# Kernel tuning notes

Measured on AMD Instinct MI355X. Metric: run time of the kernel, lower is better.

The kernel has to match this reference:

```python
import jax, jax.numpy as jnp
import numpy as np

B, S, D, H = 4, 2048, 768, 12
DH = D // H          # 64 head dim
DF = 4 * D           # 3072 FFN hidden
EPS = 1e-5


def setup_inputs() -> dict:
    key = jax.random.key(0)
    ks = jax.random.split(key, 16)
    s = 0.02
    inp = {
        "Q": jax.random.normal(ks[0], (B, S, D), jnp.float32),
        "K": jax.random.normal(ks[1], (B, S, D), jnp.float32),
        "V": jax.random.normal(ks[2], (B, S, D), jnp.float32),
        "Wq": s * jax.random.normal(ks[3], (D, D), jnp.float32),
        "bq": jnp.zeros((D,), jnp.float32),
        "Wk": s * jax.random.normal(ks[4], (D, D), jnp.float32),
        "bk": jnp.zeros((D,), jnp.float32),
        "Wv": s * jax.random.normal(ks[5], (D, D), jnp.float32),
        "bv": jnp.zeros((D,), jnp.float32),
        "Wo": s * jax.random.normal(ks[6], (D, D), jnp.float32),
        "bo": jnp.zeros((D,), jnp.float32),
        "ln_g": jnp.ones((D,), jnp.float32),
        "ln_b": jnp.zeros((D,), jnp.float32),
        "W1": s * jax.random.normal(ks[7], (D, DF), jnp.float32),
        "b1": jnp.zeros((DF,), jnp.float32),
        "W2": s * jax.random.normal(ks[8], (DF, D), jnp.float32),
        "b2": jnp.zeros((D,), jnp.float32),
    }
    return inp


def _split_heads(x):  # [B,S,D] -> [B,H,S,DH]
    return x.reshape(B, S, H, DH).transpose(0, 2, 1, 3)


def _layernorm(x, g, b):
    mu = jnp.mean(x, axis=-1, keepdims=True)
    var = jnp.mean(jnp.square(x - mu), axis=-1, keepdims=True)
    return (x - mu) * jax.lax.rsqrt(var + EPS) * g + b


def reference(Q, K, V, Wq, bq, Wk, bk, Wv, bv, Wo, bo, ln_g, ln_b, W1, b1, W2, b2):
    q = _split_heads(Q @ Wq + bq)            # [B,H,S,DH]
    k = _split_heads(K @ Wk + bk)
    v = _split_heads(V @ Wv + bv)
    scale = 1.0 / jnp.sqrt(jnp.asarray(DH, q.dtype))
    scores = jnp.einsum("bhqd,bhkd->bhqk", q, k) * scale   # [B,H,S,S]
    attn = jax.nn.softmax(scores, axis=-1)
    ctx = jnp.einsum("bhqk,bhkd->bhqd", attn, v)            # [B,H,S,DH]
    ctx = ctx.transpose(0, 2, 1, 3).reshape(B, S, D)
    attn_out = ctx @ Wo + bo
    h = _layernorm(Q + attn_out, ln_g, ln_b)                # residual + LN
    ff = jax.nn.gelu(h @ W1 + b1, approximate=False) @ W2 + b2
    return ff
```

## Files before the change

### kernel.cpp

```cpp
#include <hip/hip_runtime.h>
#include <hip/hip_bf16.h>
#include <math.h>

#define Bsz 4
#define Ssz 2048
#define Dsz 768
#define Hn  12
#define DHn 64
#define DFn 3072
#define NTOK (Bsz*Ssz)
#define EPSL 1e-5f

typedef __attribute__((ext_vector_type(8))) short bf16x8;
typedef __attribute__((ext_vector_type(4))) float f32x4;

__device__ __forceinline__ unsigned short f2bf(float f) {
    unsigned int u = __float_as_uint(f);
    u += 0x7fffu + ((u >> 16) & 1u);
    return (unsigned short)(u >> 16);
}
__device__ __forceinline__ float bf2f(unsigned short h) {
    return __uint_as_float(((unsigned int)h) << 16);
}

__device__ __forceinline__ void swizzle_mn(int bid, int mtot, int nb, int& m, int& n)
{
    const int xcd = bid & 7;
    const int idx = bid >> 3;
    m = xcd * (mtot >> 3) + idx / nb;
    n = idx % nb;
}

__global__ __launch_bounds__(256)
void wsplit_k(const float* __restrict__ W, unsigned short* __restrict__ Wh,
              unsigned short* __restrict__ Wl, int K, int N)
{
    __shared__ float tile[32][33];
    const int n0 = blockIdx.x * 32, k0 = blockIdx.y * 32;
    const int x = threadIdx.x, y = threadIdx.y;
    #pragma unroll
    for (int i = 0; i < 4; i++)
        tile[y + 8 * i][x] = W[(size_t)(k0 + y + 8 * i) * N + n0 + x];
    __syncthreads();
    #pragma unroll
    for (int i = 0; i < 4; i++) {
        float v = tile[x][y + 8 * i];
        unsigned short hb = f2bf(v);
        size_t o = (size_t)(n0 + y + 8 * i) * K + k0 + x;
        Wh[o] = hb;
        Wl[o] = f2bf(v - bf2f(hb));
    }
}

__global__ __launch_bounds__(256)
void presplit_k(const float* __restrict__ Qf, const float* __restrict__ Kf,
                const float* __restrict__ Vf,
                unsigned short* __restrict__ Qh, unsigned short* __restrict__ Ql,
                unsigned short* __restrict__ Kh, unsigned short* __restrict__ Kl,
                unsigned short* __restrict__ Vh)
{
    const int blocksPerSeg = (NTOK * Dsz) / 2048;
    const int seg = blockIdx.x / blocksPerSeg;
    const int idx = ((blockIdx.x % blocksPerSeg) * 256 + threadIdx.x) * 8;
    const float* src = (seg == 0) ? Qf : (seg == 1) ? Kf : Vf;

    float4 a = *(const float4*)(src + idx);
    float4 b = *(const float4*)(src + idx + 4);
    float fv[8] = {a.x, a.y, a.z, a.w, b.x, b.y, b.z, b.w};

    bf16x8 h8, l8;
    #pragma unroll
    for (int e = 0; e < 8; e++) {
        unsigned short hb = f2bf(fv[e]);
        h8[e] = (short)hb;
        l8[e] = (short)f2bf(fv[e] - bf2f(hb));
    }
    unsigned short* Hp = (seg == 0) ? Qh : (seg == 1) ? Kh : Vh;
    *(bf16x8*)(Hp + idx) = h8;
    if (seg < 2) {
        unsigned short* Lp = (seg == 0) ? Ql : Kl;
        *(bf16x8*)(Lp + idx) = l8;
    }
}

__global__ __launch_bounds__(256)
void qkv_mfma(const unsigned short* __restrict__ Qsh, const unsigned short* __restrict__ Qsl,
              const unsigned short* __restrict__ Ksh, const unsigned short* __restrict__ Ksl,
              const unsigned short* __restrict__ Vsh,
              const unsigned short* __restrict__ Wqh, const unsigned short* __restrict__ Wql,
              const unsigned short* __restrict__ Wkh, const unsigned short* __restrict__ Wkl,
              const unsigned short* __restrict__ Wvh, const unsigned short* __restrict__ Wvl,
              const float* __restrict__ bq, const float* __restrict__ bk,
              const float* __restrict__ bv,
              unsigned short* __restrict__ qh, unsigned short* __restrict__ ql,
              unsigned short* __restrict__ kh, unsigned short* __restrict__ kl,
              unsigned short* __restrict__ vout)
{
    __shared__ short smem[16384];
    short* As_h = smem;
    short* As_l = smem + 4096;
    short* Bs_h = smem + 8192;
    short* Bs_l = smem + 12288;

    const int t    = threadIdx.x;
    const int lane = t & 63;
    const int w    = t >> 6;
    const int wm   = w >> 1;
    const int wn   = w & 1;

    int m_tile, nblk;
    swizzle_mn(blockIdx.x, 192, 6, m_tile, nblk);
    const int which = m_tile / 64;
    const int m0    = (m_tile % 64) * 128;
    const int n0    = nblk * 128;

    const unsigned short* Ah = (which == 0) ? Qsh : (which == 1) ? Ksh : Vsh;
    const unsigned short* Al = (which == 0) ? Qsl : Ksl;
    const unsigned short* Bh = (which == 0) ? Wqh : (which == 1) ? Wkh : Wvh;
    const unsigned short* Bl = (which == 0) ? Wql : (which == 1) ? Wkl : Wvl;
    const float* bias = (which == 0) ? bq : (which == 1) ? bk : bv;

    f32x4 acc[4][4];
    #pragma unroll
    for (int i = 0; i < 4; i++)
        #pragma unroll
        for (int j = 0; j < 4; j++)
            acc[i][j] = (f32x4){0.f, 0.f, 0.f, 0.f};

    const int fr = lane & 15;
    const int q8 = (lane >> 4) * 8;

    for (int k0 = 0; k0 < Dsz; k0 += 32) {
        __syncthreads();
        #pragma unroll
        for (int it = 0; it < 2; it++) {
            const int p   = t + 256 * it;
            const int row = p >> 2;
            const int c8  = (p & 3) * 8;
            const unsigned short* ga_h = Ah + (size_t)(m0 + row) * Dsz + k0 + c8;
            const unsigned short* gb_h = Bh + (size_t)(n0 + row) * Dsz + k0 + c8;
            __builtin_amdgcn_global_load_lds((const __attribute__((address_space(1))) void*)ga_h,
                (__attribute__((address_space(3))) void*)(As_h + p * 8), 16, 0, 0);
            __builtin_amdgcn_global_load_lds((const __attribute__((address_space(1))) void*)gb_h,
                (__attribute__((address_space(3))) void*)(Bs_h + p * 8), 16, 0, 0);
            if (which < 2) {
                const unsigned short* ga_l = Al + (size_t)(m0 + row) * Dsz + k0 + c8;
                const unsigned short* gb_l = Bl + (size_t)(n0 + row) * Dsz + k0 + c8;
                __builtin_amdgcn_global_load_lds((const __attribute__((address_space(1))) void*)ga_l,
                    (__attribute__((address_space(3))) void*)(As_l + p * 8), 16, 0, 0);
                __builtin_amdgcn_global_load_lds((const __attribute__((address_space(1))) void*)gb_l,
                    (__attribute__((address_space(3))) void*)(Bs_l + p * 8), 16, 0, 0);
            }
        }
        __syncthreads();

        bf16x8 a_h[4], a_l[4], b_h[4], b_l[4];
        #pragma unroll
        for (int i = 0; i < 4; i++) {
            const int ra = (wm * 64 + i * 16 + fr) * 32 + q8;
            const int rb = (wn * 64 + i * 16 + fr) * 32 + q8;
            a_h[i] = *(const bf16x8*)&As_h[ra];
            b_h[i] = *(const bf16x8*)&Bs_h[rb];
            if (which < 2) {
                a_l[i] = *(const bf16x8*)&As_l[ra];
                b_l[i] = *(const bf16x8*)&Bs_l[rb];
            }
        }
        if (which < 2) {
            #pragma unroll
            for (int i = 0; i < 4; i++)
                #pragma unroll
                for (int j = 0; j < 4; j++) {
                    acc[i][j] = __builtin_amdgcn_mfma_f32_16x16x32_bf16(a_l[i], b_h[j], acc[i][j], 0, 0, 0);
                    acc[i][j] = __builtin_amdgcn_mfma_f32_16x16x32_bf16(a_h[i], b_l[j], acc[i][j], 0, 0, 0);
                    acc[i][j] = __builtin_amdgcn_mfma_f32_16x16x32_bf16(a_h[i], b_h[j], acc[i][j], 0, 0, 0);
                }
        } else {
            #pragma unroll
            for (int i = 0; i < 4; i++)
                #pragma unroll
                for (int j = 0; j < 4; j++)
                    acc[i][j] = __builtin_amdgcn_mfma_f32_16x16x32_bf16(a_h[i], b_h[j], acc[i][j], 0, 0, 0);
        }
    }

    const int quad = lane >> 4;
    #pragma unroll
    for (int i = 0; i < 4; i++)
        #pragma unroll
        for (int j = 0; j < 4; j++) {
            const int n  = n0 + wn * 64 + j * 16 + fr;
            const float bn = bias[n];
            const int hh = n >> 6, dh = n & 63;
            #pragma unroll
            for (int r = 0; r < 4; r++) {
                const int m = m0 + wm * 64 + i * 16 + quad * 4 + r;
                const int bb = m >> 11, s = m & 2047;
                const size_t o = (((size_t)bb * Hn + hh) * Ssz + s) * DHn + dh;
                float v = acc[i][j][r] + bn;
                unsigned short hb = f2bf(v);
                if (which == 0) { qh[o] = hb; ql[o] = f2bf(v - bf2f(hb)); }
                else if (which == 1) { kh[o] = hb; kl[o] = f2bf(v - bf2f(hb)); }
                else vout[o] = hb;
            }
        }
}

__global__ __launch_bounds__(256)
void vtrans_k(const unsigned short* __restrict__ src, unsigned short* __restrict__ dst)
{
    __shared__ unsigned short tl[32][33];
    const int s0 = blockIdx.x * 32;
    const int d0 = blockIdx.y * 32;
    const int hd = blockIdx.z;
    const int x = threadIdx.x, y = threadIdx.y;
    const size_t base = (size_t)hd * Ssz * DHn;
    #pragma unroll
    for (int i = 0; i < 4; i++)
        tl[y + 8 * i][x] = src[base + (size_t)(s0 + y + 8 * i) * DHn + d0 + x];
    __syncthreads();
    #pragma unroll
    for (int i = 0; i < 4; i++)
        dst[base + (size_t)(d0 + y + 8 * i) * Ssz + s0 + x] = tl[x][y + 8 * i];
}

template<int MODE, bool ASPLIT, bool BSPLIT>
__global__ __launch_bounds__(256)
void gemm_mfma(const unsigned short* __restrict__ Ah, const unsigned short* __restrict__ Al,
               const unsigned short* __restrict__ Bh, const unsigned short* __restrict__ Bl,
               const float* __restrict__ bias, const float* __restrict__ res,
               float* __restrict__ Cf, unsigned short* __restrict__ Cb,
               int M, int N, int K)
{
    __shared__ short smem[16384];
    short* As_h = smem;
    short* As_l = smem + 4096;
    short* Bs_h = smem + 8192;
    short* Bs_l = smem + 12288;

    const int t    = threadIdx.x;
    const int lane = t & 63;
    const int w    = t >> 6;
    const int wm   = w >> 1;
    const int wn   = w & 1;

    int mt, nt_;
    swizzle_mn(blockIdx.x, M >> 7, N >> 7, mt, nt_);
    const int m0 = mt * 128;
    const int n0 = nt_ * 128;

    f32x4 acc[4][4];
    #pragma unroll
    for (int i = 0; i < 4; i++)
        #pragma unroll
        for (int j = 0; j < 4; j++)
            acc[i][j] = (f32x4){0.f, 0.f, 0.f, 0.f};

    const int fr = lane & 15;
    const int q8 = (lane >> 4) * 8;

    for (int k0 = 0; k0 < K; k0 += 32) {
        __syncthreads();
        #pragma unroll
        for (int it = 0; it < 2; it++) {
            const int p   = t + 256 * it;
            const int row = p >> 2;
            const int c8  = (p & 3) * 8;
            const unsigned short* ga_h = Ah + (size_t)(m0 + row) * K + k0 + c8;
            const unsigned short* gb_h = Bh + (size_t)(n0 + row) * K + k0 + c8;
            __builtin_amdgcn_global_load_lds((const __attribute__((address_space(1))) void*)ga_h,
                (__attribute__((address_space(3))) void*)(As_h + p * 8), 16, 0, 0);
            if (ASPLIT) {
                const unsigned short* ga_l = Al + (size_t)(m0 + row) * K + k0 + c8;
                __builtin_amdgcn_global_load_lds((const __attribute__((address_space(1))) void*)ga_l,
                    (__attribute__((address_space(3))) void*)(As_l + p * 8), 16, 0, 0);
            }
            __builtin_amdgcn_global_load_lds((const __attribute__((address_space(1))) void*)gb_h,
                (__attribute__((address_space(3))) void*)(Bs_h + p * 8), 16, 0, 0);
            if (BSPLIT) {
                const unsigned short* gb_l = Bl + (size_t)(n0 + row) * K + k0 + c8;
                __builtin_amdgcn_global_load_lds((const __attribute__((address_space(1))) void*)gb_l,
                    (__attribute__((address_space(3))) void*)(Bs_l + p * 8), 16, 0, 0);
            }
        }
        __syncthreads();

        bf16x8 a_h[4], a_l[4], b_h[4], b_l[4];
        #pragma unroll
        for (int i = 0; i < 4; i++) {
            const int ra = (wm * 64 + i * 16 + fr) * 32 + q8;
            const int rb = (wn * 64 + i * 16 + fr) * 32 + q8;
            a_h[i] = *(const bf16x8*)&As_h[ra];
            if (ASPLIT) a_l[i] = *(const bf16x8*)&As_l[ra];
            b_h[i] = *(const bf16x8*)&Bs_h[rb];
            if (BSPLIT) b_l[i] = *(const bf16x8*)&Bs_l[rb];
        }
        #pragma unroll
        for (int i = 0; i < 4; i++)
            #pragma unroll
            for (int j = 0; j < 4; j++) {
                if (ASPLIT)
                    acc[i][j] = __builtin_amdgcn_mfma_f32_16x16x32_bf16(a_l[i], b_h[j], acc[i][j], 0, 0, 0);
                if (BSPLIT)
                    acc[i][j] = __builtin_amdgcn_mfma_f32_16x16x32_bf16(a_h[i], b_l[j], acc[i][j], 0, 0, 0);
                acc[i][j] = __builtin_amdgcn_mfma_f32_16x16x32_bf16(a_h[i], b_h[j], acc[i][j], 0, 0, 0);
            }
    }

    const int quad = lane >> 4;
    #pragma unroll
    for (int i = 0; i < 4; i++)
        #pragma unroll
        for (int j = 0; j < 4; j++) {
            const int n  = n0 + wn * 64 + j * 16 + fr;
            const float bn = bias[n];
            #pragma unroll
            for (int r = 0; r < 4; r++) {
                const int m = m0 + wm * 64 + i * 16 + quad * 4 + r;
                float v = acc[i][j][r] + bn;
                if (MODE == 1) {
                    v += res[(size_t)m * N + n];
                    Cf[(size_t)m * N + n] = v;
                } else if (MODE == 2) {
                    v = 0.5f * v * (1.0f + erff(v * 0.70710678118654752f));
                    Cb[(size_t)m * N + n] = f2bf(v);
                } else {
                    Cf[(size_t)m * N + n] = v;
                }
            }
        }
}

__device__ __forceinline__ void stage16(const unsigned short* src, short* dst,
                                        int p0, int lane, int row0, int rstride, int col0)
{
    const int p   = p0 + lane;
    const int n   = p >> 3;
    const int cst = (p & 7) ^ (n & 7);
    const unsigned short* g = src + (size_t)(row0 + n) * rstride + col0 + cst * 8;
    __builtin_amdgcn_global_load_lds((const __attribute__((address_space(1))) void*)g,
        (__attribute__((address_space(3))) void*)(dst + p0 * 8), 16, 0, 0);
}

__device__ __forceinline__ bf16x8 frag(const short* arr, int row, int c)
{
    const int pos = row * 8 + (c ^ (row & 7));
    return *(const bf16x8*)&arr[pos * 8];
}

__global__ __launch_bounds__(256)
void attn_mfma(const unsigned short* __restrict__ qh, const unsigned short* __restrict__ ql,
               const unsigned short* __restrict__ kh, const unsigned short* __restrict__ kl,
               const unsigned short* __restrict__ vt, unsigned short* __restrict__ ch)
{
    const int hid = blockIdx.x;
    const int b   = hid / Hn;
    const int h   = hid - b * Hn;
    const int q0  = blockIdx.y * 64;
    const int t    = threadIdx.x;
    const int lane = t & 63;
    const int w    = t >> 6;
    const int fr   = lane & 15;
    const int quad = lane >> 4;

    __shared__ short sKV[12288];
    __shared__ short sQP[8192];
    short* Kh_s = sKV;
    short* Kl_s = sKV + 4096;
    short* Vh_s = sKV + 8192;
    short* Qh_s = sQP;
    short* Ql_s = sQP + 4096;
    float* Pw   = (float*)sQP + w * 1024;

    const size_t hoff = (size_t)hid * Ssz * DHn;

    stage16(qh + hoff, Qh_s, w * 128,      lane, q0, DHn, 0);
    stage16(qh + hoff, Qh_s, w * 128 + 64, lane, q0, DHn, 0);
    stage16(ql + hoff, Ql_s, w * 128,      lane, q0, DHn, 0);
    stage16(ql + hoff, Ql_s, w * 128 + 64, lane, q0, DHn, 0);

    f32x4 O[4];
    #pragma unroll
    for (int d = 0; d < 4; d++) O[d] = (f32x4){0.f, 0.f, 0.f, 0.f};
    float lp[4] = {0.f, 0.f, 0.f, 0.f};

    bf16x8 qfh[2], qfl[2];
    const float scale = 0.125f;

    for (int kt = 0; kt < Ssz / 64; kt++) {
        __syncthreads();
        const int kr = kt * 64;
        #pragma unroll
        for (int bt = 0; bt < 2; bt++) {
            const int p0 = w * 128 + bt * 64;
            stage16(kh + hoff, Kh_s, p0, lane, kr, DHn, 0);
            stage16(kl + hoff, Kl_s, p0, lane, kr, DHn, 0);
            stage16(vt + hoff, Vh_s, p0, lane, 0, Ssz, kr);
        }
        __syncthreads();

        if (kt == 0) {
            #pragma unroll
            for (int kc = 0; kc < 2; kc++) {
                qfh[kc] = frag(Qh_s, w * 16 + fr, kc * 4 + quad);
                qfl[kc] = frag(Ql_s, w * 16 + fr, kc * 4 + quad);
            }
            __syncthreads();
        }

        f32x4 sc[4];
        #pragma unroll
        for (int nt = 0; nt < 4; nt++) sc[nt] = (f32x4){0.f, 0.f, 0.f, 0.f};
        #pragma unroll
        for (int nt = 0; nt < 4; nt++)
            #pragma unroll
            for (int kc = 0; kc < 2; kc++) {
                bf16x8 bh = frag(Kh_s, nt * 16 + fr, kc * 4 + quad);
                bf16x8 bl = frag(Kl_s, nt * 16 + fr, kc * 4 + quad);
                sc[nt] = __builtin_amdgcn_mfma_f32_16x16x32_bf16(qfl[kc], bh, sc[nt], 0, 0, 0);
                sc[nt] = __builtin_amdgcn_mfma_f32_16x16x32_bf16(qfh[kc], bl, sc[nt], 0, 0, 0);
                sc[nt] = __builtin_amdgcn_mfma_f32_16x16x32_bf16(qfh[kc], bh, sc[nt], 0, 0, 0);
            }

        #pragma unroll
        for (int r = 0; r < 4; r++) {
            const int m = quad * 4 + r;
            #pragma unroll
            for (int nt = 0; nt < 4; nt++) {
                float p = __expf(sc[nt][r] * scale);
                const int j  = nt * 16 + fr;
                const int c4 = j >> 2;
                Pw[(m * 16 + (c4 ^ m)) * 4 + (j & 3)] = p;
                lp[r] += p;
            }
        }

        #pragma unroll
        for (int kc = 0; kc < 2; kc++) {
            const int c4a = kc * 8 + quad * 2;
            float4 pa = *(float4*)&Pw[(fr * 16 + (c4a ^ fr)) * 4];
            float4 pb = *(float4*)&Pw[(fr * 16 + ((c4a + 1) ^ fr)) * 4];
            union { bf16x8 v; __hip_bfloat162 b2[4]; } P;
            P.b2[0] = __float22bfloat162_rn(make_float2(pa.x, pa.y));
            P.b2[1] = __float22bfloat162_rn(make_float2(pa.z, pa.w));
            P.b2[2] = __float22bfloat162_rn(make_float2(pb.x, pb.y));
            P.b2[3] = __float22bfloat162_rn(make_float2(pb.z, pb.w));
            #pragma unroll
            for (int dt = 0; dt < 4; dt++) {
                bf16x8 vh = frag(Vh_s, dt * 16 + fr, kc * 4 + quad);
                O[dt] = __builtin_amdgcn_mfma_f32_16x16x32_bf16(P.v, vh, O[dt], 0, 0, 0);
            }
        }
    }

    #pragma unroll
    for (int r = 0; r < 4; r++) {
        float ls = lp[r];
        #pragma unroll
        for (int msk = 1; msk < 16; msk <<= 1) ls += __shfl_xor(ls, msk);
        const float linv = 1.0f / ls;
        const int s = q0 + w * 16 + quad * 4 + r;
        unsigned short* och = ch + ((size_t)b * Ssz + s) * Dsz + h * DHn;
        #pragma unroll
        for (int dt = 0; dt < 4; dt++)
            och[dt * 16 + fr] = f2bf(O[dt][r] * linv);
    }
}

__global__ __launch_bounds__(256)
void ln_k(const float* __restrict__ x, const float* __restrict__ g,
          const float* __restrict__ bb, unsigned short* __restrict__ yh)
{
    const int row = blockIdx.x;
    const float* xr = x + (size_t)row * Dsz;
    unsigned short* yhr = yh + (size_t)row * Dsz;
    const int t = threadIdx.x;

    float v0 = xr[t], v1 = xr[t + 256], v2 = xr[t + 512];
    float s = v0 + v1 + v2;
    #pragma unroll
    for (int o = 1; o < 64; o <<= 1) s += __shfl_xor(s, o, 64);

    __shared__ float red1[4];
    __shared__ float red2[4];
    const int wid = t >> 6, lane = t & 63;
    if (lane == 0) red1[wid] = s;
    __syncthreads();
    const float mean = (red1[0] + red1[1] + red1[2] + red1[3]) * (1.0f / Dsz);

    float d0 = v0 - mean, d1 = v1 - mean, d2 = v2 - mean;
    float vs = d0 * d0 + d1 * d1 + d2 * d2;
    #pragma unroll
    for (int o = 1; o < 64; o <<= 1) vs += __shfl_xor(vs, o, 64);
    if (lane == 0) red2[wid] = vs;
    __syncthreads();
    const float var = (red2[0] + red2[1] + red2[2] + red2[3]) * (1.0f / Dsz);
    const float inv = rsqrtf(var + EPSL);

    yhr[t]       = f2bf(d0 * inv * g[t]       + bb[t]);
    yhr[t + 256] = f2bf(d1 * inv * g[t + 256] + bb[t + 256]);
    yhr[t + 512] = f2bf(d2 * inv * g[t + 512] + bb[t + 512]);
}

extern "C" void kernel_launch(void* const* d_in, const int* in_sizes, int n_in,
                              void* d_out, int out_size, void* d_ws, size_t ws_size,
                              hipStream_t stream)
{
    (void)in_sizes; (void)n_in; (void)out_size; (void)ws_size;
    const float* Q    = (const float*)d_in[0];
    const float* Kin  = (const float*)d_in[1];
    const float* Vin  = (const float*)d_in[2];
    const float* Wq   = (const float*)d_in[3];
    const float* bq   = (const float*)d_in[4];
    const float* Wk   = (const float*)d_in[5];
    const float* bk   = (const float*)d_in[6];
    const float* Wv   = (const float*)d_in[7];
    const float* bv   = (const float*)d_in[8];
    const float* Wo   = (const float*)d_in[9];
    const float* bo   = (const float*)d_in[10];
    const float* ln_g = (const float*)d_in[11];
    const float* ln_b = (const float*)d_in[12];
    const float* W1   = (const float*)d_in[13];
    const float* b1   = (const float*)d_in[14];
    const float* W2   = (const float*)d_in[15];
    const float* b2   = (const float*)d_in[16];
    float* out = (float*)d_out;

    const size_t NT = (size_t)NTOK * Dsz;
    unsigned short* usws = (unsigned short*)d_ws;
    unsigned short* qh  = usws + 0 * NT;
    unsigned short* ql  = usws + 1 * NT;
    unsigned short* kh  = usws + 2 * NT;
    unsigned short* kl  = usws + 3 * NT;
    unsigned short* vt  = usws + 4 * NT;
    unsigned short* ch  = usws + 6 * NT;
    unsigned short* wsp = usws + 8 * NT;
    const size_t SW = (size_t)Dsz * Dsz;
    unsigned short* Wqh = wsp + 0 * SW;
    unsigned short* Wql = wsp + 1 * SW;
    unsigned short* Wkh = wsp + 2 * SW;
    unsigned short* Wkl = wsp + 3 * SW;
    unsigned short* Wvh = wsp + 4 * SW;
    unsigned short* Wvl = wsp + 5 * SW;
    unsigned short* Woh = wsp + 6 * SW;
    unsigned short* Wol = wsp + 7 * SW;
    unsigned short* W1h = wsp + 8 * SW;
    unsigned short* W1l = wsp + 12 * SW;
    unsigned short* W2h = wsp + 16 * SW;
    unsigned short* W2l = wsp + 20 * SW;
    float*          hpre = (float*)usws;
    unsigned short* hh   = kh;
    unsigned short* hbuf = usws + 4 * NT;

    unsigned short* Qsh = usws + 4 * NT;
    unsigned short* Qsl = usws + 5 * NT;
    unsigned short* Ksh = usws + 7 * NT;
    unsigned short* Ksl = (unsigned short*)d_out;
    unsigned short* Vsh = (unsigned short*)d_out + NT;

    dim3 wb(32, 8);
    wsplit_k<<<dim3(Dsz / 32, Dsz / 32), wb, 0, stream>>>(Wq, Wqh, Wql, Dsz, Dsz);
    wsplit_k<<<dim3(Dsz / 32, Dsz / 32), wb, 0, stream>>>(Wk, Wkh, Wkl, Dsz, Dsz);
    wsplit_k<<<dim3(Dsz / 32, Dsz / 32), wb, 0, stream>>>(Wv, Wvh, Wvl, Dsz, Dsz);
    wsplit_k<<<dim3(Dsz / 32, Dsz / 32), wb, 0, stream>>>(Wo, Woh, Wol, Dsz, Dsz);
    wsplit_k<<<dim3(DFn / 32, Dsz / 32), wb, 0, stream>>>(W1, W1h, W1l, Dsz, DFn);
    wsplit_k<<<dim3(Dsz / 32, DFn / 32), wb, 0, stream>>>(W2, W2h, W2l, DFn, Dsz);

    presplit_k<<<3 * (NTOK * Dsz / 2048), 256, 0, stream>>>(
        Q, Kin, Vin, Qsh, Qsl, Ksh, Ksl, Vsh);

    qkv_mfma<<<1152, 256, 0, stream>>>(
        Qsh, Qsl, Ksh, Ksl, Vsh,
        Wqh, Wql, Wkh, Wkl, Wvh, Wvl, bq, bk, bv,
        qh, ql, kh, kl, ch);

    vtrans_k<<<dim3(Ssz / 32, DHn / 32, Bsz * Hn), wb, 0, stream>>>(ch, vt);

    attn_mfma<<<dim3(Bsz * Hn, Ssz / 64), 256, 0, stream>>>(qh, ql, kh, kl, vt, ch);

    gemm_mfma<1, false, true><<<384, 256, 0, stream>>>(
        ch, nullptr, Woh, Wol, bo, Q, hpre, nullptr, NTOK, Dsz, Dsz);

    ln_k<<<NTOK, 256, 0, stream>>>(hpre, ln_g, ln_b, hh);

    gemm_mfma<2, false, true><<<1536, 256, 0, stream>>>(
        hh, nullptr, W1h, W1l, b1, nullptr, nullptr, hbuf, NTOK, DFn, Dsz);
    gemm_mfma<3, false, false><<<384, 256, 0, stream>>>(
        hbuf, nullptr, W2h, nullptr, b2, nullptr, out, nullptr, NTOK, Dsz, DFn);
}
```

Baseline: 642.2 us.

## Process two query tiles per wave in attention to reuse K/V fragments

The attention kernel now launches 2 waves (128 threads) per 64-query block instead of 4, and each wave handles 32 query rows as two 16-row tiles. Every K and V fragment read from LDS now feeds two sets of MFMAs, which halves LDS fragment traffic per unit of MFMA work. Each wave issues twice as many global-to-LDS staging loads per tile. The trade-off is more registers per wave (doubled score, output and Q fragment arrays) and fewer waves per block to hide latency.

Result: slower. 689.5 us (+7.4%).

```diff
diff --git a/kernel.cpp b/kernel.cpp
--- a/kernel.cpp
+++ b/kernel.cpp
@@ -348,7 +348,7 @@
     return *(const bf16x8*)&arr[pos * 8];
 }
 
-__global__ __launch_bounds__(256)
+__global__ __launch_bounds__(128)
 void attn_mfma(const unsigned short* __restrict__ qh, const unsigned short* __restrict__ ql,
                const unsigned short* __restrict__ kh, const unsigned short* __restrict__ kl,
                const unsigned short* __restrict__ vt, unsigned short* __restrict__ ch)
@@ -370,29 +370,32 @@
     short* Vh_s = sKV + 8192;
     short* Qh_s = sQP;
     short* Ql_s = sQP + 4096;
-    float* Pw   = (float*)sQP + w * 1024;
+    float* Pw   = (float*)sQP + w * 2048;
 
     const size_t hoff = (size_t)hid * Ssz * DHn;
 
-    stage16(qh + hoff, Qh_s, w * 128,      lane, q0, DHn, 0);
-    stage16(qh + hoff, Qh_s, w * 128 + 64, lane, q0, DHn, 0);
-    stage16(ql + hoff, Ql_s, w * 128,      lane, q0, DHn, 0);
-    stage16(ql + hoff, Ql_s, w * 128 + 64, lane, q0, DHn, 0);
-
-    f32x4 O[4];
-    #pragma unroll
-    for (int d = 0; d < 4; d++) O[d] = (f32x4){0.f, 0.f, 0.f, 0.f};
-    float lp[4] = {0.f, 0.f, 0.f, 0.f};
-
-    bf16x8 qfh[2], qfl[2];
+    #pragma unroll
+    for (int c = 0; c < 4; c++) {
+        stage16(qh + hoff, Qh_s, w * 256 + c * 64, lane, q0, DHn, 0);
+        stage16(ql + hoff, Ql_s, w * 256 + c * 64, lane, q0, DHn, 0);
+    }
+
+    f32x4 O[2][4];
+    #pragma unroll
+    for (int qt = 0; qt < 2; qt++)
+        #pragma unroll
+        for (int d = 0; d < 4; d++) O[qt][d] = (f32x4){0.f, 0.f, 0.f, 0.f};
+    float lp[2][4] = {{0.f, 0.f, 0.f, 0.f}, {0.f, 0.f, 0.f, 0.f}};
+
+    bf16x8 qfh[2][2], qfl[2][2];
     const float scale = 0.125f;
 
     for (int kt = 0; kt < Ssz / 64; kt++) {
         __syncthreads();
         const int kr = kt * 64;
         #pragma unroll
-        for (int bt = 0; bt < 2; bt++) {
-            const int p0 = w * 128 + bt * 64;
+        for (int c = 0; c < 4; c++) {
+            const int p0 = w * 256 + c * 64;
             stage16(kh + hoff, Kh_s, p0, lane, kr, DHn, 0);
             stage16(kl + hoff, Kl_s, p0, lane, kr, DHn, 0);
             stage16(vt + hoff, Vh_s, p0, lane, 0, Ssz, kr);
@@ -401,70 +404,85 @@
 
         if (kt == 0) {
             #pragma unroll
-            for (int kc = 0; kc < 2; kc++) {
-                qfh[kc] = frag(Qh_s, w * 16 + fr, kc * 4 + quad);
-                qfl[kc] = frag(Ql_s, w * 16 + fr, kc * 4 + quad);
-            }
+            for (int qt = 0; qt < 2; qt++)
+                #pragma unroll
+                for (int kc = 0; kc < 2; kc++) {
+                    qfh[qt][kc] = frag(Qh_s, w * 32 + qt * 16 + fr, kc * 4 + quad);
+                    qfl[qt][kc] = frag(Ql_s, w * 32 + qt * 16 + fr, kc * 4 + quad);
+                }
             __syncthreads();
         }
 
-        f32x4 sc[4];
-        #pragma unroll
-        for (int nt = 0; nt < 4; nt++) sc[nt] = (f32x4){0.f, 0.f, 0.f, 0.f};
+        f32x4 sc[2][4];
+        #pragma unroll
+        for (int qt = 0; qt < 2; qt++)
+            #pragma unroll
+            for (int nt = 0; nt < 4; nt++) sc[qt][nt] = (f32x4){0.f, 0.f, 0.f, 0.f};
         #pragma unroll
         for (int nt = 0; nt < 4; nt++)
             #pragma unroll
             for (int kc = 0; kc < 2; kc++) {
                 bf16x8 bh = frag(Kh_s, nt * 16 + fr, kc * 4 + quad);
                 bf16x8 bl = frag(Kl_s, nt * 16 + fr, kc * 4 + quad);
-                sc[nt] = __builtin_amdgcn_mfma_f32_16x16x32_bf16(qfl[kc], bh, sc[nt], 0, 0, 0);
-                sc[nt] = __builtin_amdgcn_mfma_f32_16x16x32_bf16(qfh[kc], bl, sc[nt], 0, 0, 0);
-                sc[nt] = __builtin_amdgcn_mfma_f32_16x16x32_bf16(qfh[kc], bh, sc[nt], 0, 0, 0);
-            }
-
-        #pragma unroll
-        for (int r = 0; r < 4; r++) {
-            const int m = quad * 4 + r;
-            #pragma unroll
-            for (int nt = 0; nt < 4; nt++) {
-                float p = __expf(sc[nt][r] * scale);
-                const int j  = nt * 16 + fr;
-                const int c4 = j >> 2;
-                Pw[(m * 16 + (c4 ^ m)) * 4 + (j & 3)] = p;
-                lp[r] += p;
-            }
-        }
+                #pragma unroll
+                for (int qt = 0; qt < 2; qt++) {
+                    sc[qt][nt] = __builtin_amdgcn_mfma_f32_16x16x32_bf16(qfl[qt][kc], bh, sc[qt][nt], 0, 0, 0);
+                    sc[qt][nt] = __builtin_amdgcn_mfma_f32_16x16x32_bf16(qfh[qt][kc], bl, sc[qt][nt], 0, 0, 0);
+                    sc[qt][nt] = __builtin_amdgcn_mfma_f32_16x16x32_bf16(qfh[qt][kc], bh, sc[qt][nt], 0, 0, 0);
+                }
+            }
+
+        #pragma unroll
+        for (int qt = 0; qt < 2; qt++)
+            #pragma unroll
+            for (int r = 0; r < 4; r++) {
+                const int m = quad * 4 + r;
+                #pragma unroll
+                for (int nt = 0; nt < 4; nt++) {
+                    float p = __expf(sc[qt][nt][r] * scale);
+                    const int j  = nt * 16 + fr;
+                    const int c4 = j >> 2;
+                    Pw[qt * 1024 + (m * 16 + (c4 ^ m)) * 4 + (j & 3)] = p;
+                    lp[qt][r] += p;
+                }
+            }
 
         #pragma unroll
         for (int kc = 0; kc < 2; kc++) {
             const int c4a = kc * 8 + quad * 2;
-            float4 pa = *(float4*)&Pw[(fr * 16 + (c4a ^ fr)) * 4];
-            float4 pb = *(float4*)&Pw[(fr * 16 + ((c4a + 1) ^ fr)) * 4];
-            union { bf16x8 v; __hip_bfloat162 b2[4]; } P;
-            P.b2[0] = __float22bfloat162_rn(make_float2(pa.x, pa.y));
-            P.b2[1] = __float22bfloat162_rn(make_float2(pa.z, pa.w));
-            P.b2[2] = __float22bfloat162_rn(make_float2(pb.x, pb.y));
-            P.b2[3] = __float22bfloat162_rn(make_float2(pb.z, pb.w));
+            union { bf16x8 v; __hip_bfloat162 b2[4]; } P[2];
+            #pragma unroll
+            for (int qt = 0; qt < 2; qt++) {
+                float4 pa = *(float4*)&Pw[qt * 1024 + (fr * 16 + (c4a ^ fr)) * 4];
+                float4 pb = *(float4*)&Pw[qt * 1024 + (fr * 16 + ((c4a + 1) ^ fr)) * 4];
+                P[qt].b2[0] = __float22bfloat162_rn(make_float2(pa.x, pa.y));
+                P[qt].b2[1] = __float22bfloat162_rn(make_float2(pa.z, pa.w));
+                P[qt].b2[2] = __float22bfloat162_rn(make_float2(pb.x, pb.y));
+                P[qt].b2[3] = __float22bfloat162_rn(make_float2(pb.z, pb.w));
+            }
             #pragma unroll
             for (int dt = 0; dt < 4; dt++) {
                 bf16x8 vh = frag(Vh_s, dt * 16 + fr, kc * 4 + quad);
-                O[dt] = __builtin_amdgcn_mfma_f32_16x16x32_bf16(P.v, vh, O[dt], 0, 0, 0);
+                O[0][dt] = __builtin_amdgcn_mfma_f32_16x16x32_bf16(P[0].v, vh, O[0][dt], 0, 0, 0);
+                O[1][dt] = __builtin_amdgcn_mfma_f32_16x16x32_bf16(P[1].v, vh, O[1][dt], 0, 0, 0);
             }
         }
     }
 
     #pragma unroll
-    for (int r = 0; r < 4; r++) {
-        float ls = lp[r];
-        #pragma unroll
-        for (int msk = 1; msk < 16; msk <<= 1) ls += __shfl_xor(ls, msk);
-        const float linv = 1.0f / ls;
-        const int s = q0 + w * 16 + quad * 4 + r;
-        unsigned short* och = ch + ((size_t)b * Ssz + s) * Dsz + h * DHn;
-        #pragma unroll
-        for (int dt = 0; dt < 4; dt++)
-            och[dt * 16 + fr] = f2bf(O[dt][r] * linv);
-    }
+    for (int qt = 0; qt < 2; qt++)
+        #pragma unroll
+        for (int r = 0; r < 4; r++) {
+            float ls = lp[qt][r];
+            #pragma unroll
+            for (int msk = 1; msk < 16; msk <<= 1) ls += __shfl_xor(ls, msk);
+            const float linv = 1.0f / ls;
+            const int s = q0 + w * 32 + qt * 16 + quad * 4 + r;
+            unsigned short* och = ch + ((size_t)b * Ssz + s) * Dsz + h * DHn;
+            #pragma unroll
+            for (int dt = 0; dt < 4; dt++)
+                och[dt * 16 + fr] = f2bf(O[qt][dt][r] * linv);
+        }
 }
 
 __global__ __launch_bounds__(256)
@@ -576,7 +594,7 @@
 
     vtrans_k<<<dim3(Ssz / 32, DHn / 32, Bsz * Hn), wb, 0, stream>>>(ch, vt);
 
-    attn_mfma<<<dim3(Bsz * Hn, Ssz / 64), 256, 0, stream>>>(qh, ql, kh, kl, vt, ch);
+    attn_mfma<<<dim3(Bsz * Hn, Ssz / 64), 128, 0, stream>>>(qh, ql, kh, kl, vt, ch);
 
     gemm_mfma<1, false, true><<<384, 256, 0, stream>>>(
         ch, nullptr, Woh, Wol, bo, Q, hpre, nullptr, NTOK, Dsz, Dsz);
```
